# Kernel optimization log

Measured on AMD Instinct MI355X. Metric: run time of the kernel, lower is better.

Reference implementation:

```python
import jax, jax.numpy as jnp
import numpy as np

NR, K = 175, 250              # num_ranges, top_k
N = NR * K                    # 43750 active radar points
SHAPE0 = (56, 350, 512)       # (ele, range, azi) full-res sparse grid
SHAPE1 = (28, 175, 256)       # after stride-2 sparse conv
SHAPE2 = (14, 88, 128)        # after second stride-2 sparse conv
CAP1 = 350000                 # <= 8*N unique active cells after stride-2 conv
CAP2 = 69000                  # reachable region bound at stage 2 (14*88*56)
BC = 16                       # base_channel
C1, C2, CO = 2 * BC, 8 * BC, 128
OFFS = [(a, b, c) for a in range(3) for b in range(3) for c in range(3)]


def bn(x, p):
    # BatchNorm1d (eval form): p = [gamma, beta, running_mean, running_var]
    g, b, m, v = p
    return (x - m) * jax.lax.rsqrt(v + 1e-3) * g + b


def gn(x, groups, gamma, beta):
    n, c = x.shape
    xr = x.reshape(n, groups, c // groups)
    m = xr.mean(-1, keepdims=True)
    v = ((xr - m) ** 2).mean(-1, keepdims=True)
    return ((xr - m) * jax.lax.rsqrt(v + 1e-5)).reshape(n, c) * gamma + beta


def build_lut(coords, shape, n):
    # dense coord -> row-index map; out-of-bounds (padded) coords are dropped
    lut = jnp.full(shape, -1, jnp.int32)
    return lut.at[coords[:, 0], coords[:, 1], coords[:, 2]].set(jnp.arange(n, dtype=jnp.int32), mode='drop')


def subm_conv(feats, coords, lut, shape, w):
    # submanifold 3x3x3 conv: outputs only at active sites (gather-GEMM-accumulate)
    S = jnp.array(shape, jnp.int32)
    out = jnp.zeros((feats.shape[0], w.shape[-1]), feats.dtype)
    for k, off in enumerate(OFFS):
        nb = coords + (jnp.array(off, jnp.int32) - 1)
        inb = jnp.all((nb >= 0) & (nb < S), axis=-1)
        nbc = jnp.clip(nb, 0, S - 1)
        idx = lut[nbc[:, 0], nbc[:, 1], nbc[:, 2]]
        ok = inb & (idx >= 0)
        f = jnp.where(ok[:, None], feats[jnp.maximum(idx, 0)], 0.0)
        out = out + f @ w[k]
    return out


def down_conv(feats, coords_in, lut_in, shape_in, shape_out, cap, w):
    # SparseConv3d k=3 stride=2 pad=1: output sites = cells with any active input in receptive field
    mask = jnp.zeros(shape_in, bool).at[coords_in[:, 0], coords_in[:, 1], coords_in[:, 2]].set(True, mode='drop')
    pm = jnp.pad(mask, 1)
    om = jnp.zeros(shape_out, bool)
    for (a, b, c) in OFFS:
        om = om | pm[a:a + 2 * shape_out[0]:2, b:b + 2 * shape_out[1]:2, c:c + 2 * shape_out[2]:2]
    i0, i1, i2 = jnp.nonzero(om, size=cap, fill_value=0)
    oc = jnp.stack([i0, i1, i2], -1).astype(jnp.int32)
    valid = jnp.arange(cap) < om.sum()
    S = jnp.array(shape_in, jnp.int32)
    out = jnp.zeros((cap, w.shape[-1]), feats.dtype)
    for k, off in enumerate(OFFS):
        nb = 2 * oc + (jnp.array(off, jnp.int32) - 1)   # input coord = 2j + k - 1
        inb = jnp.all((nb >= 0) & (nb < S), axis=-1)
        nbc = jnp.clip(nb, 0, S - 1)
        idx = lut_in[nbc[:, 0], nbc[:, 1], nbc[:, 2]]
        ok = inb & (idx >= 0)
        f = jnp.where(ok[:, None], feats[jnp.maximum(idx, 0)], 0.0)
        out = out + f @ w[k]
    # padded (invalid) rows get out-of-bounds coords so later scatters/luts drop them
    oc_safe = jnp.where(valid[:, None], oc, jnp.array(shape_out, jnp.int32))
    return out, oc_safe


def basic_block(f, coords, lut, shape, w2, p2):
    h = jax.nn.relu(bn(subm_conv(f, coords, lut, shape, w2[0]), p2[0]))
    h = bn(subm_conv(h, coords, lut, shape, w2[1]), p2[1])
    return jax.nn.relu(h + f)


def range_attn(pw, c1, c3, ele_table, azi_table, wq, bq, wk, bk, wv, bv):
    x = pw.reshape(NR, K, 1)
    e = ele_table[c1.reshape(NR, K)]   # [NR,K,3]
    a = azi_table[c3.reshape(NR, K)]   # [NR,K,3]
    scale = 32.0 ** -0.5               # queries.size(-1) = hidden_dim = 32
    for l in range(4):
        xin = jnp.concatenate([x, e, a], -1)           # [NR,K,7]
        q = xin @ wq[l] + bq[l]
        kk = xin @ wk[l] + bk[l]
        v = xin @ wv[l] + bv[l]
        att = jax.nn.softmax(jnp.einsum('rkd,rjd->rkj', q, kk) * scale, axis=-1)
        x = jnp.einsum('rkj,rjd->rkd', att, v)         # [NR,K,1]
    return x.reshape(N, 1)


def forward(voxel_features, coors, ele_table, azi_table, wq, bq, wk, bk, wv, bv,
            w_in, b_in, gin_g, gin_b, w_d1, bn_d1, w_r1, bn_r1,
            w_d2, bn_d2, w_r2, bn_r2, w_out, b_out, gout_g, gout_b):
    c1, c2, c3 = coors[:, 1], coors[:, 2], coors[:, 3]
    pw = jnp.log10(voxel_features[:, -2])[:, None]
    f_att = range_attn(pw, c1, c3, ele_table, azi_table, wq, bq, wk, bk, wv, bv)
    ele = c1 * 2 - 9          # (56 - 37*2)//2 = -9
    rng = c2 * 2
    azi = c3 * 2 + 149        # (512 - 107*2)//2 = 149
    feats = jnp.concatenate([ele[:, None].astype(jnp.float32), rng[:, None].astype(jnp.float32),
                             azi[:, None].astype(jnp.float32), f_att], -1)   # [N,4]
    coords0 = jnp.stack([ele, rng, azi], -1).astype(jnp.int32)
    # conv_input: 1x1x1 SubMConv (per-point linear) + GroupNorm(8) + ReLU
    f0 = jax.nn.relu(gn(feats @ w_in + b_in, 8, gin_g, gin_b))
    lut0 = build_lut(coords0, SHAPE0, N)
    f1, oc1 = down_conv(f0, coords0, lut0, SHAPE0, SHAPE1, CAP1, w_d1)
    f1 = jax.nn.relu(bn(f1, bn_d1))
    lut1 = build_lut(oc1, SHAPE1, CAP1)
    f1 = basic_block(f1, oc1, lut1, SHAPE1, w_r1[0], bn_r1[0])
    f1 = basic_block(f1, oc1, lut1, SHAPE1, w_r1[1], bn_r1[1])
    f2, oc2 = down_conv(f1, oc1, lut1, SHAPE1, SHAPE2, CAP2, w_d2)
    f2 = jax.nn.relu(bn(f2, bn_d2))
    lut2 = build_lut(oc2, SHAPE2, CAP2)
    f2 = basic_block(f2, oc2, lut2, SHAPE2, w_r2[0], bn_r2[0])
    f2 = basic_block(f2, oc2, lut2, SHAPE2, w_r2[1], bn_r2[1])
    # conv_out: SubMConv3d(k=3, bias) + GroupNorm(16) + ReLU
    fo = subm_conv(f2, oc2, lut2, SHAPE2, w_out) + b_out
    fo = jax.nn.relu(gn(fo, 16, gout_g, gout_b))
    dense = jnp.zeros(SHAPE2 + (CO,), fo.dtype).at[oc2[:, 0], oc2[:, 1], oc2[:, 2]].set(fo, mode='drop')
    # torch dense: [1,C,ele,range,azi].permute(0,1,4,3,2) -> [1,C,azi,range,ele]
    return jnp.transpose(dense, (3, 2, 1, 0))[None]


def setup_inputs():
    key = jax.random.key(0)
    ks = iter(jax.random.split(key, 64))
    nrm = lambda shp, s: jax.random.normal(next(ks), shp, jnp.float32) * s

    def bnp(c):
        return jnp.stack([1.0 + nrm((c,), 0.1), nrm((c,), 0.1), nrm((c,), 0.05),
                          1.0 + 0.1 * jax.random.uniform(next(ks), (c,), jnp.float32)])

    voxel_features = jax.random.uniform(next(ks), (N, 2), jnp.float32, 0.1, 100.0)
    c0 = jnp.zeros((N,), jnp.int32)
    c1 = jax.random.randint(next(ks), (N,), 5, 33, jnp.int32)      # ele bin -> ele_ind in [1,55]
    c2 = jnp.repeat(jnp.arange(NR, dtype=jnp.int32), K)            # 250 points per range bin
    c3 = jax.random.randint(next(ks), (N,), 0, 107, jnp.int32)
    coors = jnp.stack([c0, c1, c2, c3], -1)
    return dict(
        voxel_features=voxel_features, coors=coors, batch_size=1,
        ele_table=nrm((37, 3), 1.0), azi_table=nrm((107, 3), 1.0),
        wq=nrm((4, 7, 32), 0.3), bq=nrm((4, 32), 0.1),
        wk=nrm((4, 7, 32), 0.3), bk=nrm((4, 32), 0.1),
        wv=nrm((4, 7, 1), 0.3), bv=nrm((4, 1), 0.1),
        w_in=nrm((4, BC), 0.5), b_in=nrm((BC,), 0.1),
        gin_g=1.0 + nrm((BC,), 0.1), gin_b=nrm((BC,), 0.1),
        w_d1=nrm((27, BC, C1), (27 * BC) ** -0.5), bn_d1=bnp(C1),
        w_r1=nrm((2, 2, 27, C1, C1), (27 * C1) ** -0.5),
        bn_r1=jnp.stack([jnp.stack([bnp(C1), bnp(C1)]), jnp.stack([bnp(C1), bnp(C1)])]),
        w_d2=nrm((27, C1, C2), (27 * C1) ** -0.5), bn_d2=bnp(C2),
        w_r2=nrm((2, 2, 27, C2, C2), (27 * C2) ** -0.5),
        bn_r2=jnp.stack([jnp.stack([bnp(C2), bnp(C2)]), jnp.stack([bnp(C2), bnp(C2)])]),
        w_out=nrm((27, C2, CO), (27 * C2) ** -0.5), b_out=nrm((CO,), 0.1),
        gout_g=1.0 + nrm((CO,), 0.1), gout_b=nrm((CO,), 0.1),
    )


def reference(voxel_features, coors, batch_size, ele_table, azi_table, wq, bq, wk, bk, wv, bv,
              w_in, b_in, gin_g, gin_b, w_d1, bn_d1, w_r1, bn_r1,
              w_d2, bn_d2, w_r2, bn_r2, w_out, b_out, gout_g, gout_b):
    assert batch_size == 1
    return forward(voxel_features, coors, ele_table, azi_table, wq, bq, wk, bk, wv, bv,
                   w_in, b_in, gin_g, gin_b, w_d1, bn_d1, w_r1, bn_r1,
                   w_d2, bn_d2, w_r2, bn_r2, w_out, b_out, gout_g, gout_b)
```

## Files before the change

kernel.cpp:

```cpp
#include <hip/hip_runtime.h>
#include <math.h>

#define NRR 175
#define KK 250
#define NN (NRR*KK)

#define S0_0 56
#define S0_1 350
#define S0_2 512
#define S1_0 28
#define S1_1 175
#define S1_2 256
#define S2_0 14
#define S2_1 88
#define S2_2 128
#define CAP1 350000
#define CAP2 69000
#define C1 32
#define C2 128

#define CELLS0 (S0_0*S0_1*S0_2)
#define CELLS1 (S1_0*S1_1*S1_2)
#define CELLS2 (S2_0*S2_1*S2_2)

#define ATT_SCALE 0.17677669529663687f

typedef __attribute__((ext_vector_type(8))) __bf16 bf16x8;
typedef __attribute__((ext_vector_type(16))) float f32x16;

__device__ __forceinline__ unsigned short f2b(float x) {
    unsigned int u = __builtin_bit_cast(unsigned int, x);
    unsigned int r = u + 0x7FFFu + ((u >> 16) & 1u);
    return (unsigned short)(r >> 16);
}
__device__ __forceinline__ float b2f(unsigned short h) {
    return __builtin_bit_cast(float, (unsigned int)h << 16);
}

__device__ __forceinline__ int block_incl_scan(int v, int* s) {
    int t = threadIdx.x;
    s[t] = v; __syncthreads();
    #pragma unroll
    for (int d = 1; d < 256; d <<= 1) {
        int x = (t >= d) ? s[t - d] : 0;
        __syncthreads();
        s[t] += x;
        __syncthreads();
    }
    return s[t];
}

__device__ __forceinline__ void cand(int p, int So, int* o, int& no) {
    no = 0;
    if ((p & 1) == 0) {
        int q = p >> 1; if (q < So) o[no++] = q;
    } else {
        int q = (p - 1) >> 1; if (q < So) o[no++] = q;
        q = (p + 1) >> 1;     if (q < So) o[no++] = q;
    }
}

__global__ __launch_bounds__(256) void k_init(const float* __restrict__ vf,
                                              const int* __restrict__ coors,
                                              float* __restrict__ x,
                                              int* __restrict__ lut0,
                                              int* __restrict__ om1) {
    int i = blockIdx.x * 256 + threadIdx.x;
    if (i >= NN) return;
    x[i] = log10f(vf[i * 2]);
    int c1 = coors[i * 4 + 1], c2 = coors[i * 4 + 2], c3 = coors[i * 4 + 3];
    int e = 2 * c1 - 9, rg = 2 * c2, az = 2 * c3 + 149;
    atomicMax(&lut0[(e * S0_1 + rg) * S0_2 + az], i);
    int A[2], B[2], C[2]; int na, nb, nc;
    cand(e, S1_0, A, na); cand(rg, S1_1, B, nb); cand(az, S1_2, C, nc);
    for (int ia = 0; ia < na; ia++)
        for (int ib = 0; ib < nb; ib++)
            for (int ic = 0; ic < nc; ic++)
                om1[(A[ia] * S1_1 + B[ib]) * S1_2 + C[ic]] = 1;
}

#define QS 40
__global__ __launch_bounds__(256, 1) void k_attn(float* __restrict__ x_io,
    const int* __restrict__ coors,
    const float* __restrict__ et, const float* __restrict__ at,
    const float* __restrict__ wq, const float* __restrict__ bq,
    const float* __restrict__ wk, const float* __restrict__ bk,
    const float* __restrict__ wv, const float* __restrict__ bv) {
    __shared__ float xin[KK * 7];
    __shared__ unsigned short ksh_h[256 * QS];
    __shared__ unsigned short ksh_l[256 * QS];
    __shared__ float vsh[256];
    const int r = blockIdx.x;
    const int t = threadIdx.x;
    const int w = t >> 6, ln = t & 63, l31 = ln & 31, lh = ln >> 5;

    for (int i = t; i < KK; i += 256) {
        int gi = r * KK + i;
        xin[i * 7 + 0] = x_io[gi];
        int c1 = coors[gi * 4 + 1], c3 = coors[gi * 4 + 3];
        xin[i * 7 + 1] = et[c1 * 3 + 0]; xin[i * 7 + 2] = et[c1 * 3 + 1]; xin[i * 7 + 3] = et[c1 * 3 + 2];
        xin[i * 7 + 4] = at[c3 * 3 + 0]; xin[i * 7 + 5] = at[c3 * 3 + 1]; xin[i * 7 + 6] = at[c3 * 3 + 2];
    }
    __syncthreads();

    union U8 { bf16x8 v; unsigned short u[8]; };

    for (int l = 0; l < 4; l++) {
        const float* wql = wq + l * 7 * 32; const float* bql = bq + l * 32;
        const float* wkl = wk + l * 7 * 32; const float* bkl = bk + l * 32;
        const float* wvl = wv + l * 7;      const float  bvl = bv[l];
        float qh_f[32], ql_f[32];
        if (t < KK) {
            float xi[7];
            #pragma unroll
            for (int ci = 0; ci < 7; ci++) xi[ci] = xin[t * 7 + ci];
            float av = bvl;
            #pragma unroll
            for (int ci = 0; ci < 7; ci++) av += xi[ci] * wvl[ci];
            vsh[t] = av;
            #pragma unroll
            for (int d = 0; d < 32; d++) {
                float aq = bql[d], ak = bkl[d];
                #pragma unroll
                for (int ci = 0; ci < 7; ci++) { aq += xi[ci] * wql[ci * 32 + d]; ak += xi[ci] * wkl[ci * 32 + d]; }
                aq *= ATT_SCALE;
                float h = b2f(f2b(aq));
                qh_f[d] = h; ql_f[d] = aq - h;
                unsigned short k16 = f2b(ak);
                ksh_h[t * QS + d] = k16;
                ksh_l[t * QS + d] = f2b(ak - b2f(k16));
            }
        } else {
            #pragma unroll
            for (int d = 0; d < 32; d++) {
                qh_f[d] = 0.f; ql_f[d] = 0.f;
                ksh_h[t * QS + d] = 0; ksh_l[t * QS + d] = 0;
            }
            vsh[t] = 0.f;
        }
        __syncthreads();

        U8 Bh[2][2], Bl[2][2];
        #pragma unroll
        for (int b = 0; b < 2; b++) {
            int src = b * 32 + l31;
            #pragma unroll
            for (int ks = 0; ks < 2; ks++) {
                #pragma unroll
                for (int j = 0; j < 8; j++) {
                    float h0 = __shfl(qh_f[ks * 16 + j],     src, 64);
                    float h1 = __shfl(qh_f[ks * 16 + 8 + j], src, 64);
                    float l0 = __shfl(ql_f[ks * 16 + j],     src, 64);
                    float l1 = __shfl(ql_f[ks * 16 + 8 + j], src, 64);
                    Bh[b][ks].u[j] = f2b(lh ? h1 : h0);
                    Bl[b][ks].u[j] = f2b(lh ? l1 : l0);
                }
            }
        }

        float m[2]  = {-1e30f, -1e30f};
        float den[2] = {0.f, 0.f};
        float num[2] = {0.f, 0.f};

        for (int mt = 0; mt < 8; mt++) {
            U8 Ah[2], Al[2];
            int krow = mt * 32 + l31;
            #pragma unroll
            for (int ks = 0; ks < 2; ks++) {
                Ah[ks].v = *(const bf16x8*)&ksh_h[krow * QS + ks * 16 + lh * 8];
                Al[ks].v = *(const bf16x8*)&ksh_l[krow * QS + ks * 16 + lh * 8];
            }
            float4 v4[4];
            #pragma unroll
            for (int c = 0; c < 4; c++)
                v4[c] = *(const float4*)&vsh[mt * 32 + 8 * c + 4 * lh];

            #pragma unroll
            for (int b = 0; b < 2; b++) {
                f32x16 acc;
                #pragma unroll
                for (int q = 0; q < 16; q++) acc[q] = 0.f;
                acc = __builtin_amdgcn_mfma_f32_32x32x16_bf16(Ah[0].v, Bh[b][0].v, acc, 0, 0, 0);
                acc = __builtin_amdgcn_mfma_f32_32x32x16_bf16(Ah[1].v, Bh[b][1].v, acc, 0, 0, 0);
                acc = __builtin_amdgcn_mfma_f32_32x32x16_bf16(Ah[0].v, Bl[b][0].v, acc, 0, 0, 0);
                acc = __builtin_amdgcn_mfma_f32_32x32x16_bf16(Ah[1].v, Bl[b][1].v, acc, 0, 0, 0);
                acc = __builtin_amdgcn_mfma_f32_32x32x16_bf16(Al[0].v, Bh[b][0].v, acc, 0, 0, 0);
                acc = __builtin_amdgcn_mfma_f32_32x32x16_bf16(Al[1].v, Bh[b][1].v, acc, 0, 0, 0);

                float s[16];
                #pragma unroll
                for (int rr = 0; rr < 16; rr++) {
                    s[rr] = acc[rr];
                    if (mt == 7) {
                        int key = 224 + (rr & 3) + 8 * (rr >> 2) + 4 * lh;
                        if (key >= KK) s[rr] = -1e30f;
                    }
                }
                float cm = s[0];
                #pragma unroll
                for (int rr = 1; rr < 16; rr++) cm = fmaxf(cm, s[rr]);
                cm = fmaxf(cm, __shfl_xor(cm, 32, 64));
                float mn = fmaxf(m[b], cm);
                float alpha = __expf(m[b] - mn);
                float dsum = 0.f, nsum = 0.f;
                #pragma unroll
                for (int rr = 0; rr < 16; rr++) {
                    float e = __expf(s[rr] - mn);
                    dsum += e;
                    nsum += e * ((&v4[rr >> 2].x)[rr & 3]);
                }
                den[b] = den[b] * alpha + dsum;
                num[b] = num[b] * alpha + nsum;
                m[b] = mn;
            }
        }
        __syncthreads();
        #pragma unroll
        for (int b = 0; b < 2; b++) {
            float dtot = den[b] + __shfl_xor(den[b], 32, 64);
            float ntot = num[b] + __shfl_xor(num[b], 32, 64);
            int q = (w * 2 + b) * 32 + l31;
            if (lh == 0 && q < KK) xin[q * 7] = ntot / dtot;
        }
        __syncthreads();
    }
    for (int i = t; i < KK; i += 256) x_io[r * KK + i] = xin[i * 7];
}

__global__ __launch_bounds__(256) void k_f0(const int* __restrict__ coors,
    const float* __restrict__ x,
    const float* __restrict__ w_in, const float* __restrict__ b_in,
    const float* __restrict__ gg, const float* __restrict__ gb,
    unsigned short* __restrict__ f0) {
    int i = blockIdx.x * 256 + threadIdx.x;
    if (i >= NN) return;
    int c1 = coors[i * 4 + 1], c2 = coors[i * 4 + 2], c3 = coors[i * 4 + 3];
    float fe0 = (float)(2 * c1 - 9), fe1 = (float)(2 * c2), fe2 = (float)(2 * c3 + 149), fe3 = x[i];
    float tv[16];
    #pragma unroll
    for (int c = 0; c < 16; c++)
        tv[c] = b_in[c] + fe0 * w_in[c] + fe1 * w_in[16 + c] + fe2 * w_in[32 + c] + fe3 * w_in[48 + c];
    #pragma unroll
    for (int g = 0; g < 8; g++) {
        float a = tv[2 * g], b = tv[2 * g + 1];
        float m = 0.5f * (a + b);
        float va = 0.5f * ((a - m) * (a - m) + (b - m) * (b - m));
        float inv = rsqrtf(va + 1e-5f);
        f0[i * 16 + 2 * g]     = f2b(fmaxf((a - m) * inv * gg[2 * g]     + gb[2 * g],     0.f));
        f0[i * 16 + 2 * g + 1] = f2b(fmaxf((b - m) * inv * gg[2 * g + 1] + gb[2 * g + 1], 0.f));
    }
}

__global__ __launch_bounds__(256) void k_blocksum(const int* __restrict__ om,
                                                  int* __restrict__ partials, int ncells) {
    __shared__ int sh[256];
    int t = threadIdx.x;
    int base = blockIdx.x * 1024 + t * 4;
    int s = 0;
    #pragma unroll
    for (int q = 0; q < 4; q++) s += (base + q < ncells) ? om[base + q] : 0;
    int incl = block_incl_scan(s, sh);
    if (t == 255) partials[blockIdx.x] = incl;
}

__global__ __launch_bounds__(256) void k_scanparts(int* __restrict__ partials, int nparts,
                                                   int* __restrict__ pcnt, int cap) {
    __shared__ int sh[256];
    __shared__ int tot;
    int t = threadIdx.x;
    int chunk = (nparts + 255) / 256;
    int beg = t * chunk;
    int vals[8];
    int s = 0;
    #pragma unroll
    for (int i = 0; i < 8; i++) {
        if (i < chunk) {
            int ix = beg + i;
            int x = (ix < nparts) ? partials[ix] : 0;
            vals[i] = x; s += x;
        }
    }
    int incl = block_incl_scan(s, sh);
    int excl = incl - s;
    if (t == 255) tot = incl;
    int run = excl;
    #pragma unroll
    for (int i = 0; i < 8; i++) {
        if (i < chunk) {
            int ix = beg + i;
            if (ix < nparts) { partials[ix] = run; run += vals[i]; }
        }
    }
    __syncthreads();
    if (t == 0) *pcnt = min(tot, cap);
}

__global__ __launch_bounds__(256) void k_emit(const int* __restrict__ om,
                                              const int* __restrict__ partials,
                                              int* __restrict__ oc,
                                              int ncells, int D1, int D2, int cap) {
    __shared__ int sh[256];
    int t = threadIdx.x;
    int base = blockIdx.x * 1024 + t * 4;
    int v[4]; int s = 0;
    #pragma unroll
    for (int q = 0; q < 4; q++) { v[q] = (base + q < ncells) ? om[base + q] : 0; s += v[q]; }
    int incl = block_incl_scan(s, sh);
    int run = partials[blockIdx.x] + (incl - s);
    int D12 = D1 * D2;
    #pragma unroll
    for (int q = 0; q < 4; q++) {
        if (v[q]) {
            if (run < cap) {
                int lin = base + q;
                int i0 = lin / D12;
                int r2 = lin - i0 * D12;
                int i1 = r2 / D2;
                int i2 = r2 - i1 * D2;
                oc[run * 3] = i0; oc[run * 3 + 1] = i1; oc[run * 3 + 2] = i2;
            }
            run++;
        }
    }
}

__global__ __launch_bounds__(256) void k_lutscatter(const int* __restrict__ oc,
                                                    const int* __restrict__ pc,
                                                    int* __restrict__ lut, int D1, int D2) {
    int j = blockIdx.x * 256 + threadIdx.x;
    if (j >= *pc) return;
    lut[(oc[j * 3] * D1 + oc[j * 3 + 1]) * D2 + oc[j * 3 + 2]] = j;
}

__global__ __launch_bounds__(256) void k_mask2(const int* __restrict__ oc,
                                               const int* __restrict__ pc,
                                               int* __restrict__ om) {
    int j = blockIdx.x * 256 + threadIdx.x;
    if (j >= *pc) return;
    int p0 = oc[j * 3], p1 = oc[j * 3 + 1], p2 = oc[j * 3 + 2];
    int A[2], B[2], C[2]; int na, nb, nc;
    cand(p0, S2_0, A, na); cand(p1, S2_1, B, nb); cand(p2, S2_2, C, nc);
    for (int ia = 0; ia < na; ia++)
        for (int ib = 0; ib < nb; ib++)
            for (int ic = 0; ic < nc; ic++)
                om[(A[ia] * S2_1 + B[ib]) * S2_2 + C[ic]] = 1;
}

__global__ __launch_bounds__(256) void k_prepack(const float* __restrict__ w,
        unsigned short* __restrict__ wp, int nk, int cin, int cout) {
    int tid = blockIdx.x * 256 + threadIdx.x;
    int tot = nk * cin * cout;
    if (tid >= tot) return;
    int co = tid % cout; int rest = tid / cout; int ci = rest % cin; int kk = rest / cin;
    int ks = ci >> 4, kr = ci & 15, half = kr >> 3, j = kr & 7;
    int nt = co >> 5, cl = co & 31, lane = half * 32 + cl;
    wp[((((size_t)kk * (cin >> 4) + ks) * (cout >> 5) + nt) * 64 + lane) * 8 + j] = f2b(w[tid]);
}

template<int CIN, int COUT, int SD0, int SD1, int SD2, bool DOWN, int MODE>
__global__ __launch_bounds__(256, 2)
void k_mconv(const unsigned short* __restrict__ fin, const int* __restrict__ lut,
             const int* __restrict__ oc, const int* __restrict__ pc,
             const unsigned short* __restrict__ wp,
             const float* __restrict__ p0, const float* __restrict__ p1,
             const float* __restrict__ p2,
             const unsigned short* __restrict__ res, void* __restrict__ fout_) {
    constexpr int KS = CIN / 16;
    constexpr int NT = COUT / 32;
    constexpr int SROW = CIN + 8;
    constexpr int CPR = CIN / 8;
    constexpr int TM = (COUT == 128) ? 2 : 1;
    constexpr int TN = (COUT == 128) ? 2 : 1;
    __shared__ unsigned short sA[128 * SROW];
    __shared__ int sidx[128];
    __shared__ int sc[128 * 3];

    const int n = *pc;
    const int j0 = blockIdx.x * 128;
    if (j0 >= n) return;
    const int t = threadIdx.x;
    const int w = t >> 6;
    const int ln = t & 63;
    const int l31 = ln & 31;
    const int lh = ln >> 5;
    const int rowbase = (COUT == 128) ? (w & 1) * 64 : w * 32;
    const int colt0  = (COUT == 128) ? (w >> 1) * TN : 0;

    for (int i = t; i < 128 * 3; i += 256) {
        int j = j0 + i / 3;
        sc[i] = (j < n) ? oc[j * 3 + (i % 3)] : -1000000;
    }
    __syncthreads();

    f32x16 acc[TM][TN];
    #pragma unroll
    for (int a = 0; a < TM; a++)
        #pragma unroll
        for (int b = 0; b < TN; b++)
            #pragma unroll
            for (int q = 0; q < 16; q++) acc[a][b][q] = 0.f;

    for (int k = 0; k < 27; k++) {
        const int dx = k / 9 - 1, dy = (k / 3) % 3 - 1, dz = k % 3 - 1;
        if (t < 128) {
            int x = sc[t * 3], y = sc[t * 3 + 1], z = sc[t * 3 + 2];
            if (DOWN) { x = 2 * x + dx; y = 2 * y + dy; z = 2 * z + dz; }
            else      { x += dx; y += dy; z += dz; }
            int idx = -1;
            if ((unsigned)x < (unsigned)SD0 && (unsigned)y < (unsigned)SD1 && (unsigned)z < (unsigned)SD2)
                idx = lut[(x * SD1 + y) * SD2 + z];
            sidx[t] = idx;
        }
        __syncthreads();
        #pragma unroll
        for (int it = 0; it < (128 * CPR) / 256; it++) {
            int cc = t + it * 256;
            int r = cc / CPR, c = cc % CPR;
            int idx = sidx[r];
            uint4 v = make_uint4(0, 0, 0, 0);
            if (idx >= 0) v = *(const uint4*)(fin + (size_t)idx * CIN + c * 8);
            *(uint4*)(&sA[r * SROW + c * 8]) = v;
        }
        __syncthreads();
        const unsigned short* wk = wp + (size_t)k * KS * NT * 512;
        #pragma unroll
        for (int ks = 0; ks < KS; ks++) {
            bf16x8 afr[TM], bfr[TN];
            #pragma unroll
            for (int a = 0; a < TM; a++)
                afr[a] = *(const bf16x8*)(&sA[(rowbase + a * 32 + l31) * SROW + ks * 16 + lh * 8]);
            #pragma unroll
            for (int b = 0; b < TN; b++)
                bfr[b] = *(const bf16x8*)(wk + ((size_t)(ks * NT + colt0 + b) * 64 + ln) * 8);
            #pragma unroll
            for (int a = 0; a < TM; a++)
                #pragma unroll
                for (int b = 0; b < TN; b++)
                    acc[a][b] = __builtin_amdgcn_mfma_f32_32x32x16_bf16(afr[a], bfr[b], acc[a][b], 0, 0, 0);
        }
        __syncthreads();
    }

    if (MODE != 2) {
        unsigned short* fout = (unsigned short*)fout_;
        #pragma unroll
        for (int b = 0; b < TN; b++) {
            int co = (colt0 + b) * 32 + l31;
            float g_ = p0[co], bb_ = p0[COUT + co], m_ = p0[2 * COUT + co];
            float iv = rsqrtf(p0[3 * COUT + co] + 1e-3f);
            #pragma unroll
            for (int a = 0; a < TM; a++) {
                #pragma unroll
                for (int r = 0; r < 16; r++) {
                    int jr = rowbase + a * 32 + (r & 3) + 8 * (r >> 2) + 4 * lh;
                    int j = j0 + jr;
                    if (j < n) {
                        float y = (acc[a][b][r] - m_) * iv * g_ + bb_;
                        if (MODE == 1) y += b2f(res[(size_t)j * COUT + co]);
                        fout[(size_t)j * COUT + co] = f2b(fmaxf(y, 0.f));
                    }
                }
            }
        }
    } else {
        float* dout = (float*)fout_;
        #pragma unroll
        for (int b = 0; b < TN; b++) {
            int co = (colt0 + b) * 32 + l31;
            float bias = p0[co], gg_ = p1[co], gb_ = p2[co];
            #pragma unroll
            for (int a = 0; a < TM; a++) {
                #pragma unroll
                for (int r = 0; r < 16; r++) {
                    int jr = rowbase + a * 32 + (r & 3) + 8 * (r >> 2) + 4 * lh;
                    int j = j0 + jr;
                    float y = acc[a][b][r] + bias;
                    float s = y;
                    s += __shfl_xor(s, 1, 8);
                    s += __shfl_xor(s, 2, 8);
                    s += __shfl_xor(s, 4, 8);
                    float m = s * 0.125f;
                    float d = y - m;
                    float q2 = d * d;
                    q2 += __shfl_xor(q2, 1, 8);
                    q2 += __shfl_xor(q2, 2, 8);
                    q2 += __shfl_xor(q2, 4, 8);
                    float var = q2 * 0.125f;
                    float o = fmaxf(d * rsqrtf(var + 1e-5f) * gg_ + gb_, 0.f);
                    if (j < n) {
                        int aa = sc[jr * 3], bb = sc[jr * 3 + 1], cc = sc[jr * 3 + 2];
                        dout[(((size_t)co * S2_2 + cc) * S2_1 + bb) * S2_0 + aa] = o;
                    }
                }
            }
        }
    }
}

extern "C" void kernel_launch(void* const* d_in, const int* in_sizes, int n_in,
                              void* d_out, int out_size, void* d_ws, size_t ws_size,
                              hipStream_t stream) {
    const float* vf    = (const float*)d_in[0];
    const int*   coors = (const int*)d_in[1];
    const float* et    = (const float*)d_in[3];
    const float* at    = (const float*)d_in[4];
    const float* wq    = (const float*)d_in[5];
    const float* bq    = (const float*)d_in[6];
    const float* wk_   = (const float*)d_in[7];
    const float* bk    = (const float*)d_in[8];
    const float* wv    = (const float*)d_in[9];
    const float* bv    = (const float*)d_in[10];
    const float* w_in  = (const float*)d_in[11];
    const float* b_in  = (const float*)d_in[12];
    const float* gin_g = (const float*)d_in[13];
    const float* gin_b = (const float*)d_in[14];
    const float* w_d1  = (const float*)d_in[15];
    const float* bn_d1 = (const float*)d_in[16];
    const float* w_r1  = (const float*)d_in[17];
    const float* bn_r1 = (const float*)d_in[18];
    const float* w_d2  = (const float*)d_in[19];
    const float* bn_d2 = (const float*)d_in[20];
    const float* w_r2  = (const float*)d_in[21];
    const float* bn_r2 = (const float*)d_in[22];
    const float* w_out = (const float*)d_in[23];
    const float* b_out = (const float*)d_in[24];
    const float* gout_g= (const float*)d_in[25];
    const float* gout_b= (const float*)d_in[26];

    char* ws = (char*)d_ws;
    size_t cur = 0;
    auto take = [&](size_t bytes) -> char* {
        char* p = ws + cur;
        cur += (bytes + 255) & ~(size_t)255;
        return p;
    };
    char* U = take((size_t)4194304 + (size_t)CELLS0 * 4);
    float*          x_att = (float*)U;
    unsigned short* f0    = (unsigned short*)(U + 262144);
    int*            lut0  = (int*)(U + 4194304);
    unsigned short* fB1   = (unsigned short*)U;
    unsigned short* fA2   = (unsigned short*)U;
    unsigned short* fB2   = (unsigned short*)(U + 17694720);

    int*   om1      = (int*)take((size_t)CELLS1 * 4);
    int*   om2      = (int*)take((size_t)CELLS2 * 4);
    int*   partials = (int*)take(8192);
    int*   cnt      = (int*)take(256);
    int*   oc1      = (int*)take((size_t)CAP1 * 3 * 4);
    int*   oc2      = (int*)take((size_t)CAP2 * 3 * 4);
    unsigned short* fA1 = (unsigned short*)take((size_t)CAP1 * C1 * 2);
    int*   lut1     = (int*)take((size_t)CELLS1 * 4);
    int*   lut2     = (int*)take((size_t)CELLS2 * 4);
    unsigned short* wp_d1  = (unsigned short*)take((size_t)27 * 16 * 32 * 2);
    unsigned short* wp_r1  = (unsigned short*)take((size_t)108 * 32 * 32 * 2);
    unsigned short* wp_d2  = (unsigned short*)take((size_t)27 * 32 * 128 * 2);
    unsigned short* wp_r2  = (unsigned short*)take((size_t)108 * 128 * 128 * 2);
    unsigned short* wp_out = (unsigned short*)take((size_t)27 * 128 * 128 * 2);

    hipMemsetAsync(d_out, 0, (size_t)out_size * 4, stream);
    hipMemsetAsync(lut0, 0xFF, (size_t)CELLS0 * 4, stream);
    hipMemsetAsync(om1, 0, (size_t)CELLS1 * 4, stream);
    hipMemsetAsync(om2, 0, (size_t)CELLS2 * 4, stream);
    hipMemsetAsync(lut1, 0xFF, (size_t)CELLS1 * 4, stream);
    hipMemsetAsync(lut2, 0xFF, (size_t)CELLS2 * 4, stream);

    const int gN  = (NN + 255) / 256;
    const int gB1 = CELLS1 / 1024;
    const int gB2 = CELLS2 / 1024;
    const int gM1 = (CAP1 + 127) / 128;
    const int gM2 = (CAP2 + 127) / 128;
    const int gS1 = (CAP1 + 255) / 256;
    const int gS2 = (CAP2 + 255) / 256;

    k_prepack<<<(27*16*32   + 255)/256, 256, 0, stream>>>(w_d1,  wp_d1, 27, 16, 32);
    k_prepack<<<(108*32*32  + 255)/256, 256, 0, stream>>>(w_r1,  wp_r1, 108, 32, 32);
    k_prepack<<<(27*32*128  + 255)/256, 256, 0, stream>>>(w_d2,  wp_d2, 27, 32, 128);
    k_prepack<<<(108*128*128+ 255)/256, 256, 0, stream>>>(w_r2,  wp_r2, 108, 128, 128);
    k_prepack<<<(27*128*128 + 255)/256, 256, 0, stream>>>(w_out, wp_out, 27, 128, 128);

    k_init<<<gN, 256, 0, stream>>>(vf, coors, x_att, lut0, om1);
    k_attn<<<NRR, 256, 0, stream>>>(x_att, coors, et, at, wq, bq, wk_, bk, wv, bv);
    k_f0<<<gN, 256, 0, stream>>>(coors, x_att, w_in, b_in, gin_g, gin_b, f0);

    k_blocksum<<<gB1, 256, 0, stream>>>(om1, partials, CELLS1);
    k_scanparts<<<1, 256, 0, stream>>>(partials, gB1, cnt, CAP1);
    k_emit<<<gB1, 256, 0, stream>>>(om1, partials, oc1, CELLS1, S1_1, S1_2, CAP1);

    k_mconv<16, 32, S0_0, S0_1, S0_2, true, 0><<<gM1, 256, 0, stream>>>(
        f0, lut0, oc1, cnt, wp_d1, bn_d1, nullptr, nullptr, nullptr, fA1);
    k_lutscatter<<<gS1, 256, 0, stream>>>(oc1, cnt, lut1, S1_1, S1_2);

    k_mconv<32, 32, S1_0, S1_1, S1_2, false, 0><<<gM1, 256, 0, stream>>>(
        fA1, lut1, oc1, cnt, wp_r1 + 0 * 27648, bn_r1 + 0 * 128, nullptr, nullptr, nullptr, fB1);
    k_mconv<32, 32, S1_0, S1_1, S1_2, false, 1><<<gM1, 256, 0, stream>>>(
        fB1, lut1, oc1, cnt, wp_r1 + 1 * 27648, bn_r1 + 1 * 128, nullptr, nullptr, fA1, fA1);
    k_mconv<32, 32, S1_0, S1_1, S1_2, false, 0><<<gM1, 256, 0, stream>>>(
        fA1, lut1, oc1, cnt, wp_r1 + 2 * 27648, bn_r1 + 2 * 128, nullptr, nullptr, nullptr, fB1);
    k_mconv<32, 32, S1_0, S1_1, S1_2, false, 1><<<gM1, 256, 0, stream>>>(
        fB1, lut1, oc1, cnt, wp_r1 + 3 * 27648, bn_r1 + 3 * 128, nullptr, nullptr, fA1, fA1);

    k_mask2<<<gS1, 256, 0, stream>>>(oc1, cnt, om2);
    k_blocksum<<<gB2, 256, 0, stream>>>(om2, partials, CELLS2);
    k_scanparts<<<1, 256, 0, stream>>>(partials, gB2, cnt + 1, CAP2);
    k_emit<<<gB2, 256, 0, stream>>>(om2, partials, oc2, CELLS2, S2_1, S2_2, CAP2);

    k_mconv<32, 128, S1_0, S1_1, S1_2, true, 0><<<gM2, 256, 0, stream>>>(
        fA1, lut1, oc2, cnt + 1, wp_d2, bn_d2, nullptr, nullptr, nullptr, fA2);
    k_lutscatter<<<gS2, 256, 0, stream>>>(oc2, cnt + 1, lut2, S2_1, S2_2);

    const size_t wr2s = (size_t)27 * 128 * 128;
    k_mconv<128, 128, S2_0, S2_1, S2_2, false, 0><<<gM2, 256, 0, stream>>>(
        fA2, lut2, oc2, cnt + 1, wp_r2 + 0 * wr2s, bn_r2 + 0 * 512, nullptr, nullptr, nullptr, fB2);
    k_mconv<128, 128, S2_0, S2_1, S2_2, false, 1><<<gM2, 256, 0, stream>>>(
        fB2, lut2, oc2, cnt + 1, wp_r2 + 1 * wr2s, bn_r2 + 1 * 512, nullptr, nullptr, fA2, fA2);
    k_mconv<128, 128, S2_0, S2_1, S2_2, false, 0><<<gM2, 256, 0, stream>>>(
        fA2, lut2, oc2, cnt + 1, wp_r2 + 2 * wr2s, bn_r2 + 2 * 512, nullptr, nullptr, nullptr, fB2);
    k_mconv<128, 128, S2_0, S2_1, S2_2, false, 1><<<gM2, 256, 0, stream>>>(
        fB2, lut2, oc2, cnt + 1, wp_r2 + 3 * wr2s, bn_r2 + 3 * 512, nullptr, nullptr, fA2, fA2);

    k_mconv<128, 128, S2_0, S2_1, S2_2, false, 2><<<gM2, 256, 0, stream>>>(
        fA2, lut2, oc2, cnt + 1, wp_out, b_out, gout_g, gout_b, nullptr, (float*)d_out);
}
```

Measured before the change: 1.207 ms.

## Prefetch next-offset gather in registers, reshape warp tiling, scatter output via separate pass

The sparse-conv kernel now has each thread own half a row. It looks up the LUT index two offsets ahead and loads the next offset's gathered features into registers while MFMAs run, which removes the sidx/sc shared buffers and one barrier per offset. For 128-channel outputs each warp now covers all 128 rows for one 32-column tile instead of a 2x2 tile, and the min-blocks launch bound is dropped. The final conv writes a channel-major compact buffer, and a new scatter kernel fills the dense output through lut2, replacing the memset and strided scattered writes. The cost is higher register pressure, which may lower occupancy, plus an extra full pass over the dense output.

```diff
diff --git a/kernel.cpp b/kernel.cpp
--- a/kernel.cpp
+++ b/kernel.cpp
@@ -18,6 +18,7 @@
 #define CAP2 69000
 #define C1 32
 #define C2 128
+#define FOP 69632
 
 #define CELLS0 (S0_0*S0_1*S0_2)
 #define CELLS1 (S1_0*S1_1*S1_2)
@@ -358,7 +359,7 @@
 }
 
 template<int CIN, int COUT, int SD0, int SD1, int SD2, bool DOWN, int MODE>
-__global__ __launch_bounds__(256, 2)
+__global__ __launch_bounds__(256)
 void k_mconv(const unsigned short* __restrict__ fin, const int* __restrict__ lut,
              const int* __restrict__ oc, const int* __restrict__ pc,
              const unsigned short* __restrict__ wp,
@@ -369,132 +370,134 @@
     constexpr int NT = COUT / 32;
     constexpr int SROW = CIN + 8;
     constexpr int CPR = CIN / 8;
-    constexpr int TM = (COUT == 128) ? 2 : 1;
-    constexpr int TN = (COUT == 128) ? 2 : 1;
+    constexpr int HC  = CPR / 2;
+    constexpr int TM  = (COUT == 128) ? 4 : 1;
     __shared__ unsigned short sA[128 * SROW];
-    __shared__ int sidx[128];
-    __shared__ int sc[128 * 3];
 
     const int n = *pc;
     const int j0 = blockIdx.x * 128;
     if (j0 >= n) return;
     const int t = threadIdx.x;
-    const int w = t >> 6;
-    const int ln = t & 63;
-    const int l31 = ln & 31;
-    const int lh = ln >> 5;
-    const int rowbase = (COUT == 128) ? (w & 1) * 64 : w * 32;
-    const int colt0  = (COUT == 128) ? (w >> 1) * TN : 0;
-
-    for (int i = t; i < 128 * 3; i += 256) {
-        int j = j0 + i / 3;
-        sc[i] = (j < n) ? oc[j * 3 + (i % 3)] : -1000000;
-    }
-    __syncthreads();
-
-    f32x16 acc[TM][TN];
+    const int w = t >> 6, ln = t & 63, l31 = ln & 31, lh = ln >> 5;
+    const int rowb = (COUT == 128) ? 0 : w * 32;
+    const int colt = (COUT == 128) ? w : 0;
+
+    const int srow = t >> 1;
+    int cxs, cys, czs;
+    {
+        int j = j0 + srow;
+        if (j < n) { cxs = oc[j * 3]; cys = oc[j * 3 + 1]; czs = oc[j * 3 + 2]; }
+        else       { cxs = -1000000; cys = -1000000; czs = -1000000; }
+    }
+    const uint4* fin4 = (const uint4*)fin;
+
+    auto lookup = [&](int kk) -> int {
+        int dx = kk / 9 - 1, dy = (kk / 3) % 3 - 1, dz = kk % 3 - 1;
+        int x, y, z;
+        if (DOWN) { x = 2 * cxs + dx; y = 2 * cys + dy; z = 2 * czs + dz; }
+        else      { x = cxs + dx; y = cys + dy; z = czs + dz; }
+        if ((unsigned)x < (unsigned)SD0 && (unsigned)y < (unsigned)SD1 && (unsigned)z < (unsigned)SD2)
+            return lut[(x * SD1 + y) * SD2 + z];
+        return -1;
+    };
+
+    uint4 ld[HC];
+    auto loadrow = [&](int idx) {
+        #pragma unroll
+        for (int q = 0; q < HC; q++) {
+            uint4 v = make_uint4(0, 0, 0, 0);
+            if (idx >= 0) v = fin4[(size_t)idx * CPR + (t & 1) * HC + q];
+            ld[q] = v;
+        }
+    };
+
+    f32x16 acc[TM];
     #pragma unroll
     for (int a = 0; a < TM; a++)
         #pragma unroll
-        for (int b = 0; b < TN; b++)
-            #pragma unroll
-            for (int q = 0; q < 16; q++) acc[a][b][q] = 0.f;
+        for (int q = 0; q < 16; q++) acc[a][q] = 0.f;
+
+    int idxA = lookup(0);
+    loadrow(idxA);
+    int idxB = lookup(1);
 
     for (int k = 0; k < 27; k++) {
-        const int dx = k / 9 - 1, dy = (k / 3) % 3 - 1, dz = k % 3 - 1;
-        if (t < 128) {
-            int x = sc[t * 3], y = sc[t * 3 + 1], z = sc[t * 3 + 2];
-            if (DOWN) { x = 2 * x + dx; y = 2 * y + dy; z = 2 * z + dz; }
-            else      { x += dx; y += dy; z += dz; }
-            int idx = -1;
-            if ((unsigned)x < (unsigned)SD0 && (unsigned)y < (unsigned)SD1 && (unsigned)z < (unsigned)SD2)
-                idx = lut[(x * SD1 + y) * SD2 + z];
-            sidx[t] = idx;
-        }
         __syncthreads();
         #pragma unroll
-        for (int it = 0; it < (128 * CPR) / 256; it++) {
-            int cc = t + it * 256;
-            int r = cc / CPR, c = cc % CPR;
-            int idx = sidx[r];
-            uint4 v = make_uint4(0, 0, 0, 0);
-            if (idx >= 0) v = *(const uint4*)(fin + (size_t)idx * CIN + c * 8);
-            *(uint4*)(&sA[r * SROW + c * 8]) = v;
-        }
+        for (int q = 0; q < HC; q++)
+            *(uint4*)&sA[srow * SROW + ((t & 1) * HC + q) * 8] = ld[q];
         __syncthreads();
+        if (k < 26) {
+            loadrow(idxB);
+            idxB = lookup(k + 2 <= 26 ? k + 2 : 26);
+        }
         const unsigned short* wk = wp + (size_t)k * KS * NT * 512;
         #pragma unroll
         for (int ks = 0; ks < KS; ks++) {
-            bf16x8 afr[TM], bfr[TN];
-            #pragma unroll
-            for (int a = 0; a < TM; a++)
-                afr[a] = *(const bf16x8*)(&sA[(rowbase + a * 32 + l31) * SROW + ks * 16 + lh * 8]);
-            #pragma unroll
-            for (int b = 0; b < TN; b++)
-                bfr[b] = *(const bf16x8*)(wk + ((size_t)(ks * NT + colt0 + b) * 64 + ln) * 8);
-            #pragma unroll
-            for (int a = 0; a < TM; a++)
-                #pragma unroll
-                for (int b = 0; b < TN; b++)
-                    acc[a][b] = __builtin_amdgcn_mfma_f32_32x32x16_bf16(afr[a], bfr[b], acc[a][b], 0, 0, 0);
-        }
-        __syncthreads();
-    }
-
+            bf16x8 bfr = *(const bf16x8*)(wk + ((size_t)(ks * NT + colt) * 64 + ln) * 8);
+            #pragma unroll
+            for (int a = 0; a < TM; a++) {
+                bf16x8 afr = *(const bf16x8*)(&sA[(rowb + a * 32 + l31) * SROW + ks * 16 + lh * 8]);
+                acc[a] = __builtin_amdgcn_mfma_f32_32x32x16_bf16(afr, bfr, acc[a], 0, 0, 0);
+            }
+        }
+    }
+
+    const int co = colt * 32 + l31;
     if (MODE != 2) {
         unsigned short* fout = (unsigned short*)fout_;
-        #pragma unroll
-        for (int b = 0; b < TN; b++) {
-            int co = (colt0 + b) * 32 + l31;
-            float g_ = p0[co], bb_ = p0[COUT + co], m_ = p0[2 * COUT + co];
-            float iv = rsqrtf(p0[3 * COUT + co] + 1e-3f);
-            #pragma unroll
-            for (int a = 0; a < TM; a++) {
-                #pragma unroll
-                for (int r = 0; r < 16; r++) {
-                    int jr = rowbase + a * 32 + (r & 3) + 8 * (r >> 2) + 4 * lh;
-                    int j = j0 + jr;
-                    if (j < n) {
-                        float y = (acc[a][b][r] - m_) * iv * g_ + bb_;
-                        if (MODE == 1) y += b2f(res[(size_t)j * COUT + co]);
-                        fout[(size_t)j * COUT + co] = f2b(fmaxf(y, 0.f));
-                    }
+        float g_ = p0[co], bb_ = p0[COUT + co], m_ = p0[2 * COUT + co];
+        float iv = rsqrtf(p0[3 * COUT + co] + 1e-3f);
+        #pragma unroll
+        for (int a = 0; a < TM; a++) {
+            #pragma unroll
+            for (int r = 0; r < 16; r++) {
+                int j = j0 + rowb + a * 32 + (r & 3) + 8 * (r >> 2) + 4 * lh;
+                if (j < n) {
+                    float y = (acc[a][r] - m_) * iv * g_ + bb_;
+                    if (MODE == 1) y += b2f(res[(size_t)j * COUT + co]);
+                    fout[(size_t)j * COUT + co] = f2b(fmaxf(y, 0.f));
                 }
             }
         }
     } else {
-        float* dout = (float*)fout_;
-        #pragma unroll
-        for (int b = 0; b < TN; b++) {
-            int co = (colt0 + b) * 32 + l31;
-            float bias = p0[co], gg_ = p1[co], gb_ = p2[co];
-            #pragma unroll
-            for (int a = 0; a < TM; a++) {
-                #pragma unroll
-                for (int r = 0; r < 16; r++) {
-                    int jr = rowbase + a * 32 + (r & 3) + 8 * (r >> 2) + 4 * lh;
-                    int j = j0 + jr;
-                    float y = acc[a][b][r] + bias;
-                    float s = y;
-                    s += __shfl_xor(s, 1, 8);
-                    s += __shfl_xor(s, 2, 8);
-                    s += __shfl_xor(s, 4, 8);
-                    float m = s * 0.125f;
-                    float d = y - m;
-                    float q2 = d * d;
-                    q2 += __shfl_xor(q2, 1, 8);
-                    q2 += __shfl_xor(q2, 2, 8);
-                    q2 += __shfl_xor(q2, 4, 8);
-                    float var = q2 * 0.125f;
-                    float o = fmaxf(d * rsqrtf(var + 1e-5f) * gg_ + gb_, 0.f);
-                    if (j < n) {
-                        int aa = sc[jr * 3], bb = sc[jr * 3 + 1], cc = sc[jr * 3 + 2];
-                        dout[(((size_t)co * S2_2 + cc) * S2_1 + bb) * S2_0 + aa] = o;
-                    }
-                }
-            }
-        }
-    }
+        float* fo_t = (float*)fout_;
+        float bias = p0[co], gg_ = p1[co], gb_ = p2[co];
+        #pragma unroll
+        for (int a = 0; a < TM; a++) {
+            #pragma unroll
+            for (int r = 0; r < 16; r++) {
+                int j = j0 + a * 32 + (r & 3) + 8 * (r >> 2) + 4 * lh;
+                float y = acc[a][r] + bias;
+                float s = y;
+                s += __shfl_xor(s, 1, 8);
+                s += __shfl_xor(s, 2, 8);
+                s += __shfl_xor(s, 4, 8);
+                float m = s * 0.125f;
+                float d = y - m;
+                float q2 = d * d;
+                q2 += __shfl_xor(q2, 1, 8);
+                q2 += __shfl_xor(q2, 2, 8);
+                q2 += __shfl_xor(q2, 4, 8);
+                float var = q2 * 0.125f;
+                float o = fmaxf(d * rsqrtf(var + 1e-5f) * gg_ + gb_, 0.f);
+                fo_t[(size_t)co * FOP + j] = o;
+            }
+        }
+    }
+}
+
+__global__ __launch_bounds__(256) void k_scatter(const float* __restrict__ fo_t,
+                                                 const int* __restrict__ lut2,
+                                                 float* __restrict__ dout) {
+    int gid = blockIdx.x * 256 + threadIdx.x;
+    int aa = gid % S2_0; int r = gid / S2_0;
+    int bb = r % S2_1;   r /= S2_1;
+    int cc = r % S2_2;   int co = r / S2_2;
+    int idx = lut2[(aa * S2_1 + bb) * S2_2 + cc];
+    float v = 0.f;
+    if (idx >= 0) v = fo_t[(size_t)co * FOP + idx];
+    dout[gid] = v;
 }
 
 extern "C" void kernel_launch(void* const* d_in, const int* in_sizes, int n_in,
@@ -534,13 +537,16 @@
         cur += (bytes + 255) & ~(size_t)255;
         return p;
     };
-    char* U = take((size_t)4194304 + (size_t)CELLS0 * 4);
+    size_t usz1 = (size_t)4194304 + (size_t)CELLS0 * 4;
+    size_t usz2 = (size_t)17694720 + (size_t)128 * FOP * 4;
+    char* U = take(usz1 > usz2 ? usz1 : usz2);
     float*          x_att = (float*)U;
     unsigned short* f0    = (unsigned short*)(U + 262144);
     int*            lut0  = (int*)(U + 4194304);
     unsigned short* fB1   = (unsigned short*)U;
     unsigned short* fA2   = (unsigned short*)U;
     unsigned short* fB2   = (unsigned short*)(U + 17694720);
+    float*          fo_t  = (float*)(U + 17694720);
 
     int*   om1      = (int*)take((size_t)CELLS1 * 4);
     int*   om2      = (int*)take((size_t)CELLS2 * 4);
@@ -557,7 +563,6 @@
     unsigned short* wp_r2  = (unsigned short*)take((size_t)108 * 128 * 128 * 2);
     unsigned short* wp_out = (unsigned short*)take((size_t)27 * 128 * 128 * 2);
 
-    hipMemsetAsync(d_out, 0, (size_t)out_size * 4, stream);
     hipMemsetAsync(lut0, 0xFF, (size_t)CELLS0 * 4, stream);
     hipMemsetAsync(om1, 0, (size_t)CELLS1 * 4, stream);
     hipMemsetAsync(om2, 0, (size_t)CELLS2 * 4, stream);
@@ -619,5 +624,6 @@
         fB2, lut2, oc2, cnt + 1, wp_r2 + 3 * wr2s, bn_r2 + 3 * 512, nullptr, nullptr, fA2, fA2);
 
     k_mconv<128, 128, S2_0, S2_1, S2_2, false, 2><<<gM2, 256, 0, stream>>>(
-        fA2, lut2, oc2, cnt + 1, wp_out, b_out, gout_g, gout_b, nullptr, (float*)d_out);
-}
+        fA2, lut2, oc2, cnt + 1, wp_out, b_out, gout_g, gout_b, nullptr, fo_t);
+    k_scatter<<<(S2_0 * S2_1 * S2_2 * 128) / 256, 256, 0, stream>>>(fo_t, lut2, (float*)d_out);
+}
```

New measurement: 1.093 ms. -9.5%, faster.
